# Kernel optimization log

Hardware: AMD Instinct MI355X
Metric: run time of the kernel (lower is better)

The kernel has to match this reference:

```python
import jax, jax.numpy as jnp
import numpy as np

D = 1024        # d_model
H = 16          # query heads
HKV = 4         # kv heads (GQA)
HD = D // H     # head dim = 64
MAX_T = 1024
EPS = 1e-6
CAP = 50.0      # logit softcap


def _rope_cache(max_t, hd):
    inv = 1.0 / (10000.0 ** (np.arange(0, hd, 2, dtype=np.float32) / hd))  # (hd/2,)
    t = np.arange(max_t, dtype=np.float32)
    f = np.outer(t, inv)                                                   # (max_t, hd/2)
    return jnp.asarray(np.cos(f)), jnp.asarray(np.sin(f))


def setup_inputs() -> dict:
    key = jax.random.key(0)
    ks = jax.random.split(key, 5)
    x = jax.random.normal(ks[0], (2, 64, 256, D), jnp.float32)  # (B,T,S,D)
    wq = jax.random.normal(ks[1], (D, H * HD), jnp.float32) * 0.02
    wk = jax.random.normal(ks[2], (D, HKV * HD), jnp.float32) * 0.02
    wv = jax.random.normal(ks[3], (D, HKV * HD), jnp.float32) * 0.02
    wo = jax.random.normal(ks[4], (H * HD, D), jnp.float32) * 0.02
    q_scale = jnp.ones((HD,), jnp.float32)  # QKNorm learnable gains
    k_scale = jnp.ones((HD,), jnp.float32)
    rope_cos, rope_sin = _rope_cache(MAX_T, HD)
    return {"x": x, "wq": wq, "wk": wk, "wv": wv, "wo": wo,
            "q_scale": q_scale, "k_scale": k_scale,
            "rope_cos": rope_cos, "rope_sin": rope_sin}


def _rmsnorm(v, scale):
    return v * jax.lax.rsqrt(jnp.mean(v * v, axis=-1, keepdims=True) + EPS) * scale


def reference(x, wq, wk, wv, wo, q_scale, k_scale, rope_cos, rope_sin):
    B, T, S, Dm = x.shape
    # fold spatial positions into batch: each position attends causally over time
    xt = x.transpose(0, 2, 1, 3).reshape(B * S, T, Dm)          # (N,T,D)
    q = (xt @ wq).reshape(B * S, T, H, HD)
    k = (xt @ wk).reshape(B * S, T, HKV, HD)
    v = (xt @ wv).reshape(B * S, T, HKV, HD)
    # QK-norm (RMSNorm over head_dim) before RoPE
    q = _rmsnorm(q, q_scale)
    k = _rmsnorm(k, k_scale)
    # 1D RoPE over temporal positions (split-half convention)
    cos = rope_cos[:T][None, :, None, :]                        # (1,T,1,HD/2)
    sin = rope_sin[:T][None, :, None, :]

    def rot(u):
        u1, u2 = jnp.split(u, 2, axis=-1)
        return jnp.concatenate([u1 * cos - u2 * sin, u1 * sin + u2 * cos], axis=-1)

    q = rot(q)
    k = rot(k)
    # GQA: expand kv heads to match query heads
    rep = H // HKV
    k = jnp.repeat(k, rep, axis=2)
    v = jnp.repeat(v, rep, axis=2)
    scores = jnp.einsum('nthd,nshd->nhts', q, k) / np.float32(np.sqrt(HD))
    scores = CAP * jnp.tanh(scores / CAP)                        # logit softcap
    causal = jnp.tril(jnp.ones((T, T), bool))
    scores = jnp.where(causal, scores, jnp.float32(-1e30))
    a = jax.nn.softmax(scores, axis=-1)
    o = jnp.einsum('nhts,nshd->nthd', a, v).reshape(B * S, T, H * HD) @ wo
    return o.reshape(B, S, T, Dm).transpose(0, 2, 1, 3)          # (B,T,S,D)
```

## Files before the change

### kernel.cpp

```cpp
#include <hip/hip_runtime.h>
#include <hip/hip_bf16.h>

#define DM   1024
#define NHQ  16
#define NKVH 4
#define HDIM 64
#define TTT  64
#define SSS  256
#define NBB  2
#define MROWS 32768

using short8 = __attribute__((ext_vector_type(8))) short;
using short4v = __attribute__((ext_vector_type(4))) short;
using f32x4  = __attribute__((ext_vector_type(4))) float;

__device__ __forceinline__ short f2bf(float f) {
  union { __hip_bfloat16 h; short s; } u;
  u.h = __float2bfloat16(f);
  return u.s;
}

__device__ __forceinline__ f32x4 mfma16(short8 a, short8 b, f32x4 c) {
  return __builtin_amdgcn_mfma_f32_16x16x32_bf16(a, b, c, 0, 0, 0);
}

__device__ __forceinline__ void gload_lds16(const void* g, void* l) {
  __builtin_amdgcn_global_load_lds(
      (const __attribute__((address_space(1))) void*)g,
      (__attribute__((address_space(3))) void*)l, 16, 0, 0);
}

__global__ __launch_bounds__(256) void k_wt(const float* __restrict__ w,
                                            short* __restrict__ wt, int cols) {
  __shared__ float tile[32][33];
  int ctiles = cols >> 5;
  int tj = blockIdx.x % ctiles;
  int td = blockIdx.x / ctiles;
  int lx = threadIdx.x & 31, ly = threadIdx.x >> 5;
  #pragma unroll
  for (int rr = 0; rr < 32; rr += 8)
    tile[rr + ly][lx] = w[(size_t)(td * 32 + rr + ly) * cols + tj * 32 + lx];
  __syncthreads();
  #pragma unroll
  for (int rr = 0; rr < 32; rr += 8)
    wt[(size_t)(tj * 32 + rr + ly) * 1024 + td * 32 + lx] = f2bf(tile[lx][rr + ly]);
}

#define GEMM256_8PH(Ab, Bb)                                                    \
  const int tid = threadIdx.x, lane = tid & 63, wid = tid >> 6;                \
  const int wr = wid >> 2, wc = wid & 3;                                       \
  const int ln15 = lane & 15, lhi = lane >> 4;                                 \
  const int rsw = ln15 & 7;                                                    \
  f32x4 acc[8][4] = {};                                                        \
  auto SHALF = [&](const short* gb, short* lb, int half, int kt) {             \
    _Pragma("unroll")                                                          \
    for (int i = 0; i < 2; ++i) {                                              \
      int c = i * 512 + tid;                                                   \
      int row = c >> 3, slot = c & 7;                                          \
      gload_lds16(gb + (size_t)(half * 128 + row) * 1024 + kt                  \
                     + ((slot ^ (row & 7)) << 3),                              \
                  lb + half * 8192 + c * 8);                                   \
    }                                                                          \
  };                                                                           \
  SHALF(Ab, sm, 0, 0); SHALF(Ab, sm, 1, 0);                                    \
  SHALF(Bb, sm + 16384, 0, 0); SHALF(Bb, sm + 16384, 1, 0);                    \
  SHALF(Ab, sm + 32768, 0, 64); SHALF(Ab, sm + 32768, 1, 64);                  \
  SHALF(Bb, sm + 49152, 0, 64); SHALF(Bb, sm + 49152, 1, 64);                  \
  asm volatile("s_waitcnt vmcnt(8)" ::: "memory");                             \
  __builtin_amdgcn_s_barrier();                                                \
  for (int g = 0; g < 16; ++g) {                                               \
    short* cA = sm + (g & 1) * 32768;                                          \
    short* cB = cA + 16384;                                                    \
    short* nA = sm + ((g + 1) & 1) * 32768;                                    \
    const bool iA = (g > 0) && (g < 15);                                       \
    const bool iB = (g < 14);                                                  \
    short8 a[4], b0[4], b1[4];                                                 \
    _Pragma("unroll")                                                          \
    for (int n = 0; n < 4; ++n)                                                \
      b0[n] = *(const short8*)(cB + (wc * 64 + n * 16 + ln15) * 64             \
                                  + ((lhi ^ rsw) << 3));                       \
    _Pragma("unroll")                                                          \
    for (int m = 0; m < 4; ++m)                                                \
      a[m] = *(const short8*)(cA + (wr * 128 + m * 16 + ln15) * 64             \
                                 + ((lhi ^ rsw) << 3));                        \
    if (iA) SHALF(Ab, nA, 0, (g + 1) * 64);                                    \
    __builtin_amdgcn_s_barrier();                                              \
    asm volatile("s_waitcnt lgkmcnt(0)" ::: "memory");                         \
    __builtin_amdgcn_s_setprio(1);                                             \
    _Pragma("unroll")                                                          \
    for (int m = 0; m < 4; ++m)                                                \
      _Pragma("unroll")                                                        \
      for (int n = 0; n < 4; ++n) acc[m][n] = mfma16(a[m], b0[n], acc[m][n]);  \
    __builtin_amdgcn_s_setprio(0);                                             \
    __builtin_amdgcn_s_barrier();                                              \
    _Pragma("unroll")                                                          \
    for (int m = 0; m < 4; ++m)                                                \
      a[m] = *(const short8*)(cA + (wr * 128 + 64 + m * 16 + ln15) * 64        \
                                 + ((lhi ^ rsw) << 3));                        \
    if (iA) SHALF(Ab, nA, 1, (g + 1) * 64);                                    \
    __builtin_amdgcn_s_barrier();                                              \
    asm volatile("s_waitcnt lgkmcnt(0)" ::: "memory");                         \
    __builtin_amdgcn_s_setprio(1);                                             \
    _Pragma("unroll")                                                          \
    for (int m = 0; m < 4; ++m)                                                \
      _Pragma("unroll")                                                        \
      for (int n = 0; n < 4; ++n)                                              \
        acc[4 + m][n] = mfma16(a[m], b0[n], acc[4 + m][n]);                    \
    __builtin_amdgcn_s_setprio(0);                                             \
    __builtin_amdgcn_s_barrier();                                              \
    _Pragma("unroll")                                                          \
    for (int n = 0; n < 4; ++n)                                                \
      b1[n] = *(const short8*)(cB + (wc * 64 + n * 16 + ln15) * 64             \
                                  + (((4 + lhi) ^ rsw) << 3));                 \
    _Pragma("unroll")                                                          \
    for (int m = 0; m < 4; ++m)                                                \
      a[m] = *(const short8*)(cA + (wr * 128 + m * 16 + ln15) * 64             \
                                 + (((4 + lhi) ^ rsw) << 3));                  \
    __builtin_amdgcn_s_barrier();                                              \
    asm volatile("s_waitcnt lgkmcnt(0)" ::: "memory");                         \
    __builtin_amdgcn_s_setprio(1);                                             \
    _Pragma("unroll")                                                          \
    for (int m = 0; m < 4; ++m)                                                \
      _Pragma("unroll")                                                        \
      for (int n = 0; n < 4; ++n) acc[m][n] = mfma16(a[m], b1[n], acc[m][n]);  \
    __builtin_amdgcn_s_setprio(0);                                             \
    __builtin_amdgcn_s_barrier();                                              \
    _Pragma("unroll")                                                          \
    for (int m = 0; m < 4; ++m)                                                \
      a[m] = *(const short8*)(cA + (wr * 128 + 64 + m * 16 + ln15) * 64        \
                                 + (((4 + lhi) ^ rsw) << 3));                  \
    if (iB) { SHALF(Bb, cB, 0, (g + 2) * 64); SHALF(Bb, cB, 1, (g + 2) * 64); }\
    __builtin_amdgcn_s_barrier();                                              \
    asm volatile("s_waitcnt lgkmcnt(0)" ::: "memory");                         \
    __builtin_amdgcn_s_setprio(1);                                             \
    _Pragma("unroll")                                                          \
    for (int m = 0; m < 4; ++m)                                                \
      _Pragma("unroll")                                                        \
      for (int n = 0; n < 4; ++n)                                              \
        acc[4 + m][n] = mfma16(a[m], b1[n], acc[4 + m][n]);                    \
    __builtin_amdgcn_s_setprio(0);                                             \
    if (g < 14)       asm volatile("s_waitcnt vmcnt(4)" ::: "memory");         \
    else if (g == 14) asm volatile("s_waitcnt vmcnt(0)" ::: "memory");         \
    __builtin_amdgcn_s_barrier();                                              \
  }

__global__ __launch_bounds__(512) void k_qkv(
    const float* __restrict__ x, const short* __restrict__ wt,
    const float* __restrict__ qscale, const float* __restrict__ kscale,
    const float* __restrict__ rcos, const float* __restrict__ rsin,
    short* __restrict__ qb, short* __restrict__ kb, short* __restrict__ vb) {
  __shared__ __align__(16) short sm[65536];
  const int bid = blockIdx.x;
  const int swz = (bid & 7) * 96 + (bid >> 3);
  const int tn = swz % 6, tm = swz / 6;
  const short* Bb = wt + (size_t)tn * 256 * 1024;
  const int tid = threadIdx.x, lane = tid & 63, wid = tid >> 6;
  const int wr = wid >> 2, wc = wid & 3;
  const int ln15 = lane & 15, lhi = lane >> 4;
  const int rsw = ln15 & 7;
  f32x4 acc[8][4] = {};
  const int arow = tid >> 3, aslot = tid & 7;
  const float* aptr[2][2];
  #pragma unroll
  for (int half = 0; half < 2; ++half)
    #pragma unroll
    for (int i = 0; i < 2; ++i) {
      int row = half * 128 + i * 64 + arow;
      int gr = tm * 256 + row;
      int nseq = gr >> 6, t = gr & 63;
      int b = nseq >> 8, s = nseq & 255;
      aptr[half][i] = x + ((size_t)((b * 64 + t) * 256 + s)) * 1024
                        + ((aslot ^ (row & 7)) << 3);
    }
  float4 ra[2][2][2], rb[2][2][2];
  auto A_ISSUE = [&](float4 (&rg)[2][2][2], int half, int kt) {
    #pragma unroll
    for (int i = 0; i < 2; ++i) {
      rg[half][i][0] = *(const float4*)(aptr[half][i] + kt);
      rg[half][i][1] = *(const float4*)(aptr[half][i] + kt + 4);
    }
  };
  auto A_WRITE = [&](float4 (&rg)[2][2][2], short* dA, int half) {
    #pragma unroll
    for (int i = 0; i < 2; ++i) {
      short8 v;
      #pragma unroll
      for (int e = 0; e < 4; ++e) {
        v[e]     = f2bf(rg[half][i][0][e]);
        v[4 + e] = f2bf(rg[half][i][1][e]);
      }
      *(short8*)(dA + half * 8192 + (i * 512 + tid) * 8) = v;
    }
  };
  auto BHALF = [&](short* lb, int half, int kt) {
    #pragma unroll
    for (int i = 0; i < 2; ++i) {
      int c = i * 512 + tid;
      int row = c >> 3, slot = c & 7;
      gload_lds16(Bb + (size_t)(half * 128 + row) * 1024 + kt
                     + ((slot ^ (row & 7)) << 3),
                  lb + half * 8192 + c * 8);
    }
  };
  A_ISSUE(ra, 0, 0); A_ISSUE(ra, 1, 0);
  BHALF(sm + 16384, 0, 0); BHALF(sm + 16384, 1, 0);
  A_ISSUE(rb, 0, 64); A_ISSUE(rb, 1, 64);
  BHALF(sm + 49152, 0, 64); BHALF(sm + 49152, 1, 64);
  asm volatile("s_waitcnt vmcnt(16)" ::: "memory");
  A_WRITE(ra, sm, 0); A_WRITE(ra, sm, 1);
  asm volatile("s_waitcnt vmcnt(4)" ::: "memory");
  A_WRITE(rb, sm + 32768, 0); A_WRITE(rb, sm + 32768, 1);
  asm volatile("s_waitcnt lgkmcnt(0)" ::: "memory");
  __builtin_amdgcn_s_barrier();
  for (int g = 0; g < 16; ++g) {
    short* cA = sm + (g & 1) * 32768;
    short* cB = cA + 16384;
    short* nA = sm + ((g + 1) & 1) * 32768;
    const bool iA = (g > 0) && (g < 15);
    const bool iB = (g < 14);
    short8 a[4], b0[4], b1[4];
    #pragma unroll
    for (int n = 0; n < 4; ++n)
      b0[n] = *(const short8*)(cB + (wc * 64 + n * 16 + ln15) * 64 + ((lhi ^ rsw) << 3));
    #pragma unroll
    for (int m = 0; m < 4; ++m)
      a[m] = *(const short8*)(cA + (wr * 128 + m * 16 + ln15) * 64 + ((lhi ^ rsw) << 3));
    if (iA) A_ISSUE(ra, 0, (g + 1) * 64);
    __builtin_amdgcn_s_barrier();
    asm volatile("s_waitcnt lgkmcnt(0)" ::: "memory");
    __builtin_amdgcn_s_setprio(1);
    #pragma unroll
    for (int m = 0; m < 4; ++m)
      #pragma unroll
      for (int n = 0; n < 4; ++n) acc[m][n] = mfma16(a[m], b0[n], acc[m][n]);
    __builtin_amdgcn_s_setprio(0);
    __builtin_amdgcn_s_barrier();
    #pragma unroll
    for (int m = 0; m < 4; ++m)
      a[m] = *(const short8*)(cA + (wr * 128 + 64 + m * 16 + ln15) * 64 + ((lhi ^ rsw) << 3));
    if (iA) A_ISSUE(ra, 1, (g + 1) * 64);
    __builtin_amdgcn_s_barrier();
    asm volatile("s_waitcnt lgkmcnt(0)" ::: "memory");
    __builtin_amdgcn_s_setprio(1);
    #pragma unroll
    for (int m = 0; m < 4; ++m)
      #pragma unroll
      for (int n = 0; n < 4; ++n) acc[4 + m][n] = mfma16(a[m], b0[n], acc[4 + m][n]);
    __builtin_amdgcn_s_setprio(0);
    __builtin_amdgcn_s_barrier();
    #pragma unroll
    for (int n = 0; n < 4; ++n)
      b1[n] = *(const short8*)(cB + (wc * 64 + n * 16 + ln15) * 64 + (((4 + lhi) ^ rsw) << 3));
    #pragma unroll
    for (int m = 0; m < 4; ++m)
      a[m] = *(const short8*)(cA + (wr * 128 + m * 16 + ln15) * 64 + (((4 + lhi) ^ rsw) << 3));
    if (iB) { BHALF(cB, 0, (g + 2) * 64); BHALF(cB, 1, (g + 2) * 64); }
    __builtin_amdgcn_s_barrier();
    asm volatile("s_waitcnt lgkmcnt(0)" ::: "memory");
    __builtin_amdgcn_s_setprio(1);
    #pragma unroll
    for (int m = 0; m < 4; ++m)
      #pragma unroll
      for (int n = 0; n < 4; ++n) acc[m][n] = mfma16(a[m], b1[n], acc[m][n]);
    __builtin_amdgcn_s_setprio(0);
    __builtin_amdgcn_s_barrier();
    #pragma unroll
    for (int m = 0; m < 4; ++m)
      a[m] = *(const short8*)(cA + (wr * 128 + 64 + m * 16 + ln15) * 64 + (((4 + lhi) ^ rsw) << 3));
    __builtin_amdgcn_s_barrier();
    asm volatile("s_waitcnt lgkmcnt(0)" ::: "memory");
    __builtin_amdgcn_s_setprio(1);
    #pragma unroll
    for (int m = 0; m < 4; ++m)
      #pragma unroll
      for (int n = 0; n < 4; ++n) acc[4 + m][n] = mfma16(a[m], b1[n], acc[4 + m][n]);
    __builtin_amdgcn_s_setprio(0);
    if (g < 14)       asm volatile("s_waitcnt vmcnt(4)" ::: "memory");
    else if (g == 14) asm volatile("s_waitcnt vmcnt(0)" ::: "memory");
    if (iA) {
      A_WRITE(ra, nA, 0); A_WRITE(ra, nA, 1);
      asm volatile("s_waitcnt lgkmcnt(0)" ::: "memory");
    }
    __builtin_amdgcn_s_barrier();
  }

  short* ot = sm;
  if (tn < 5) {
    const float* scale = (tn < 4) ? qscale : kscale;
    float sc[4];
    #pragma unroll
    for (int n = 0; n < 4; ++n) sc[n] = scale[n * 16 + ln15];
    #pragma unroll
    for (int m = 0; m < 8; ++m) {
      #pragma unroll
      for (int j = 0; j < 4; ++j) {
        float ss = 0.f;
        #pragma unroll
        for (int n = 0; n < 4; ++n) { float v = acc[m][n][j]; ss += v * v; }
        #pragma unroll
        for (int off = 8; off; off >>= 1) ss += __shfl_xor(ss, off, 64);
        float rms = rsqrtf(ss * (1.f / 64.f) + 1e-6f);
        int rl = wr * 128 + m * 16 + lhi * 4 + j;
        int t = (tm * 256 + rl) & 63;
        #pragma unroll
        for (int n = 0; n < 2; ++n) {
          int i = n * 16 + ln15;
          float cs = rcos[t * 32 + i], sn = rsin[t * 32 + i];
          float v1 = acc[m][n][j] * rms * sc[n];
          float v2 = acc[m][n + 2][j] * rms * sc[n + 2];
          ot[rl * 256 + wc * 64 + i]      = f2bf(v1 * cs - v2 * sn);
          ot[rl * 256 + wc * 64 + i + 32] = f2bf(v1 * sn + v2 * cs);
        }
      }
    }
  } else {
    #pragma unroll
    for (int m = 0; m < 8; ++m)
      #pragma unroll
      for (int n = 0; n < 4; ++n)
        #pragma unroll
        for (int j = 0; j < 4; ++j) {
          int rl = wr * 128 + m * 16 + lhi * 4 + j;
          ot[rl * 256 + wc * 64 + n * 16 + ln15] = f2bf(acc[m][n][j]);
        }
  }
  __syncthreads();
  {
    int row = tid >> 1, half = tid & 1;
    int r = tm * 256 + row;
    const uint4* src = (const uint4*)(ot + row * 256 + half * 128);
    short* dst;
    if (tn < 4)       dst = qb + (size_t)r * 1024 + tn * 256 + half * 128;
    else if (tn == 4) dst = kb + (size_t)r * 256 + half * 128;
    else              dst = vb + (size_t)r * 256 + half * 128;
    uint4* d4 = (uint4*)dst;
    #pragma unroll
    for (int i = 0; i < 16; ++i) d4[i] = src[i];
  }
}

__global__ __launch_bounds__(512) void k_attn(const short* __restrict__ qb,
                                              const short* __restrict__ kb,
                                              const short* __restrict__ vb,
                                              short* __restrict__ ob) {
  __shared__ __align__(16) short Vt[256 * 72];
  __shared__ __align__(16) short Ps[8][64 * 72];
  const int n = blockIdx.x;
  const int tid = threadIdx.x, lane = tid & 63, wid = tid >> 6;
  const int ln15 = lane & 15, lhi = lane >> 4;
  #pragma unroll
  for (int it = 0; it < 4; ++it) {
    int id = it * 512 + tid;
    int s = id >> 5, c8 = id & 31;
    short8 vv = *(const short8*)(vb + ((size_t)(n * 64 + s)) * 256 + c8 * 8);
    #pragma unroll
    for (int e = 0; e < 8; ++e) Vt[(c8 * 8 + e) * 72 + s] = vv[e];
  }
  __syncthreads();
  short* Pt = &Ps[wid][0];
  #pragma unroll
  for (int hh = 0; hh < 2; ++hh) {
    const int h = wid + hh * 8;
    const int kvh = h >> 2;
    short8 bk[4][2], aq[4][2];
    #pragma unroll
    for (int m = 0; m < 4; ++m)
      #pragma unroll
      for (int kk = 0; kk < 2; ++kk)
        bk[m][kk] = *(const short8*)(kb + ((size_t)(n * 64 + m * 16 + ln15)) * 256
                                        + kvh * 64 + kk * 32 + lhi * 8);
    #pragma unroll
    for (int nn = 0; nn < 4; ++nn)
      #pragma unroll
      for (int kk = 0; kk < 2; ++kk)
        aq[nn][kk] = *(const short8*)(qb + ((size_t)(n * 64 + nn * 16 + ln15)) * 1024
                                         + h * 64 + kk * 32 + lhi * 8);
    f32x4 sa[4][4] = {};
    __builtin_amdgcn_s_setprio(1);
    #pragma unroll
    for (int kk = 0; kk < 2; ++kk)
      #pragma unroll
      for (int m = 0; m < 4; ++m)
        #pragma unroll
        for (int nn = 0; nn < 4; ++nn)
          sa[m][nn] = mfma16(bk[m][kk], aq[nn][kk], sa[m][nn]);
    __builtin_amdgcn_s_setprio(0);
    #pragma unroll
    for (int m = 0; m < 4; ++m)
      #pragma unroll
      for (int nn = 0; nn < 4; ++nn)
        #pragma unroll
        for (int j = 0; j < 4; ++j) {
          float e2 = __expf(sa[m][nn][j] * 0.005f);
          float cap = 50.f * (e2 - 1.f) * __builtin_amdgcn_rcpf(e2 + 1.f);
          int scur = m * 16 + lhi * 4 + j, tcur = nn * 16 + ln15;
          sa[m][nn][j] = (scur <= tcur) ? cap : -1e30f;
        }
    float inv[4];
    #pragma unroll
    for (int nn = 0; nn < 4; ++nn) {
      float mx = -3e38f;
      #pragma unroll
      for (int m = 0; m < 4; ++m)
        #pragma unroll
        for (int j = 0; j < 4; ++j) mx = fmaxf(mx, sa[m][nn][j]);
      mx = fmaxf(mx, __shfl_xor(mx, 16, 64));
      mx = fmaxf(mx, __shfl_xor(mx, 32, 64));
      float sum = 0.f;
      #pragma unroll
      for (int m = 0; m < 4; ++m)
        #pragma unroll
        for (int j = 0; j < 4; ++j) {
          float e = __expf(sa[m][nn][j] - mx);
          sa[m][nn][j] = e; sum += e;
        }
      sum += __shfl_xor(sum, 16, 64);
      sum += __shfl_xor(sum, 32, 64);
      inv[nn] = __builtin_amdgcn_rcpf(sum);
    }
    #pragma unroll
    for (int nn = 0; nn < 4; ++nn)
      #pragma unroll
      for (int m = 0; m < 4; ++m) {
        short4v w;
        #pragma unroll
        for (int j = 0; j < 4; ++j) w[j] = f2bf(sa[m][nn][j] * inv[nn]);
        *(short4v*)(Pt + (nn * 16 + ln15) * 72 + m * 16 + lhi * 4) = w;
      }
    short8 ap[4][2], bv[4][2];
    #pragma unroll
    for (int m = 0; m < 4; ++m)
      #pragma unroll
      for (int kk = 0; kk < 2; ++kk)
        ap[m][kk] = *(const short8*)(Pt + (m * 16 + ln15) * 72 + kk * 32 + lhi * 8);
    #pragma unroll
    for (int nn = 0; nn < 4; ++nn)
      #pragma unroll
      for (int kk = 0; kk < 2; ++kk)
        bv[nn][kk] = *(const short8*)(&Vt[(kvh * 64 + nn * 16 + ln15) * 72 + kk * 32 + lhi * 8]);
    f32x4 oa[4][4] = {};
    __builtin_amdgcn_s_setprio(1);
    #pragma unroll
    for (int kk = 0; kk < 2; ++kk)
      #pragma unroll
      for (int m = 0; m < 4; ++m)
        #pragma unroll
        for (int nn = 0; nn < 4; ++nn)
          oa[m][nn] = mfma16(ap[m][kk], bv[nn][kk], oa[m][nn]);
    __builtin_amdgcn_s_setprio(0);
    #pragma unroll
    for (int m = 0; m < 4; ++m)
      #pragma unroll
      for (int nn = 0; nn < 4; ++nn)
        #pragma unroll
        for (int j = 0; j < 4; ++j)
          Pt[(m * 16 + lhi * 4 + j) * 72 + nn * 16 + ln15] = f2bf(oa[m][nn][j]);
    #pragma unroll
    for (int c = 0; c < 8; ++c)
      *(uint4*)(ob + ((size_t)(n * 64 + lane)) * 1024 + h * 64 + c * 8)
          = *(const uint4*)(Pt + lane * 72 + c * 8);
  }
}

__global__ __launch_bounds__(512, 2) void k_out(const short* __restrict__ ab,
                                                const short* __restrict__ wt,
                                                float* __restrict__ out) {
  __shared__ __align__(16) short sm[65536];
  const int bid = blockIdx.x;
  const int swz = (bid & 7) * 64 + (bid >> 3);
  const int tn = swz & 3, tm = swz >> 2;
  const short* Ab = ab + (size_t)tm * 256 * 1024;
  const short* Bb = wt + (size_t)tn * 256 * 1024;
  GEMM256_8PH(Ab, Bb)

  float* of = (float*)sm;
  #pragma unroll
  for (int ch = 0; ch < 2; ++ch) {
    if (wr == ch) {
      #pragma unroll
      for (int m = 0; m < 8; ++m)
        #pragma unroll
        for (int n = 0; n < 4; ++n)
          #pragma unroll
          for (int j = 0; j < 4; ++j)
            of[(m * 16 + lhi * 4 + j) * 256 + wc * 64 + n * 16 + ln15] = acc[m][n][j];
    }
    __syncthreads();
    {
      int row = tid >> 2, q4 = tid & 3;
      int r = tm * 256 + ch * 128 + row;
      int nseq = r >> 6, t = r & 63;
      int b = nseq >> 8, s = nseq & 255;
      float* dst = out + ((size_t)((b * TTT + t) * SSS + s)) * DM + tn * 256 + q4 * 64;
      const float4* src = (const float4*)(of + row * 256 + q4 * 64);
      float4* d4 = (float4*)dst;
      #pragma unroll
      for (int i = 0; i < 16; ++i) d4[i] = src[i];
    }
    __syncthreads();
  }
}

extern "C" void kernel_launch(void* const* d_in, const int* in_sizes, int n_in,
                              void* d_out, int out_size, void* d_ws, size_t ws_size,
                              hipStream_t stream) {
  const float* x  = (const float*)d_in[0];
  const float* wq = (const float*)d_in[1];
  const float* wk = (const float*)d_in[2];
  const float* wv = (const float*)d_in[3];
  const float* wo = (const float*)d_in[4];
  const float* qs = (const float*)d_in[5];
  const float* ks = (const float*)d_in[6];
  const float* rc = (const float*)d_in[7];
  const float* rs = (const float*)d_in[8];
  float* out = (float*)d_out;
  char* ws = (char*)d_ws;

  short* ob    = (short*)(ws);
  short* wqkvT = (short*)(ws + 67108864);
  short* woT   = (short*)(ws + 70254592);
  short* qb    = (short*)(ws + 72351744);
  short* kb    = (short*)(ws + 139460608);
  short* vb    = (short*)(ws + 156237824);

  k_wt<<<1024, 256, 0, stream>>>(wq, wqkvT, 1024);
  k_wt<<<256, 256, 0, stream>>>(wk, wqkvT + (size_t)1024 * 1024, 256);
  k_wt<<<256, 256, 0, stream>>>(wv, wqkvT + (size_t)1280 * 1024, 256);
  k_wt<<<1024, 256, 0, stream>>>(wo, woT, 1024);
  k_qkv<<<768, 512, 0, stream>>>(x, wqkvT, qs, ks, rc, rs, qb, kb, vb);
  k_attn<<<512, 512, 0, stream>>>(qb, kb, vb, ob);
  k_out<<<512, 512, 0, stream>>>(ob, woT, out);
}
```

Measured before the change: 356.8 us.

## Pre-convert x to bf16 in a separate pass and reuse shared GEMM macro

```diff
diff --git a/kernel.cpp b/kernel.cpp
--- a/kernel.cpp
+++ b/kernel.cpp
@@ -28,6 +28,19 @@
   __builtin_amdgcn_global_load_lds(
       (const __attribute__((address_space(1))) void*)g,
       (__attribute__((address_space(3))) void*)l, 16, 0, 0);
+}
+
+__global__ __launch_bounds__(256) void k_xconv(const float* __restrict__ x,
+                                               short* __restrict__ xb) {
+  int r = blockIdx.x;
+  int n = r >> 6, t = r & 63;
+  int b = n >> 8, s = n & 255;
+  const float4* src = (const float4*)(x + ((size_t)((b * TTT + t) * SSS + s)) * DM);
+  short4* dst = (short4*)(xb + (size_t)r * DM);
+  float4 v = src[threadIdx.x];
+  short4 o;
+  o.x = f2bf(v.x); o.y = f2bf(v.y); o.z = f2bf(v.z); o.w = f2bf(v.w);
+  dst[threadIdx.x] = o;
 }
 
 __global__ __launch_bounds__(256) void k_wt(const float* __restrict__ w,
@@ -144,8 +157,8 @@
     __builtin_amdgcn_s_barrier();                                              \
   }
 
-__global__ __launch_bounds__(512) void k_qkv(
-    const float* __restrict__ x, const short* __restrict__ wt,
+__global__ __launch_bounds__(512, 2) void k_qkv(
+    const short* __restrict__ xb, const short* __restrict__ wt,
     const float* __restrict__ qscale, const float* __restrict__ kscale,
     const float* __restrict__ rcos, const float* __restrict__ rsin,
     short* __restrict__ qb, short* __restrict__ kb, short* __restrict__ vb) {
@@ -153,136 +166,9 @@
   const int bid = blockIdx.x;
   const int swz = (bid & 7) * 96 + (bid >> 3);
   const int tn = swz % 6, tm = swz / 6;
+  const short* Ab = xb + (size_t)tm * 256 * 1024;
   const short* Bb = wt + (size_t)tn * 256 * 1024;
-  const int tid = threadIdx.x, lane = tid & 63, wid = tid >> 6;
-  const int wr = wid >> 2, wc = wid & 3;
-  const int ln15 = lane & 15, lhi = lane >> 4;
-  const int rsw = ln15 & 7;
-  f32x4 acc[8][4] = {};
-  const int arow = tid >> 3, aslot = tid & 7;
-  const float* aptr[2][2];
-  #pragma unroll
-  for (int half = 0; half < 2; ++half)
-    #pragma unroll
-    for (int i = 0; i < 2; ++i) {
-      int row = half * 128 + i * 64 + arow;
-      int gr = tm * 256 + row;
-      int nseq = gr >> 6, t = gr & 63;
-      int b = nseq >> 8, s = nseq & 255;
-      aptr[half][i] = x + ((size_t)((b * 64 + t) * 256 + s)) * 1024
-                        + ((aslot ^ (row & 7)) << 3);
-    }
-  float4 ra[2][2][2], rb[2][2][2];
-  auto A_ISSUE = [&](float4 (&rg)[2][2][2], int half, int kt) {
-    #pragma unroll
-    for (int i = 0; i < 2; ++i) {
-      rg[half][i][0] = *(const float4*)(aptr[half][i] + kt);
-      rg[half][i][1] = *(const float4*)(aptr[half][i] + kt + 4);
-    }
-  };
-  auto A_WRITE = [&](float4 (&rg)[2][2][2], short* dA, int half) {
-    #pragma unroll
-    for (int i = 0; i < 2; ++i) {
-      short8 v;
-      #pragma unroll
-      for (int e = 0; e < 4; ++e) {
-        v[e]     = f2bf(rg[half][i][0][e]);
-        v[4 + e] = f2bf(rg[half][i][1][e]);
-      }
-      *(short8*)(dA + half * 8192 + (i * 512 + tid) * 8) = v;
-    }
-  };
-  auto BHALF = [&](short* lb, int half, int kt) {
-    #pragma unroll
-    for (int i = 0; i < 2; ++i) {
-      int c = i * 512 + tid;
-      int row = c >> 3, slot = c & 7;
-      gload_lds16(Bb + (size_t)(half * 128 + row) * 1024 + kt
-                     + ((slot ^ (row & 7)) << 3),
-                  lb + half * 8192 + c * 8);
-    }
-  };
-  A_ISSUE(ra, 0, 0); A_ISSUE(ra, 1, 0);
-  BHALF(sm + 16384, 0, 0); BHALF(sm + 16384, 1, 0);
-  A_ISSUE(rb, 0, 64); A_ISSUE(rb, 1, 64);
-  BHALF(sm + 49152, 0, 64); BHALF(sm + 49152, 1, 64);
-  asm volatile("s_waitcnt vmcnt(16)" ::: "memory");
-  A_WRITE(ra, sm, 0); A_WRITE(ra, sm, 1);
-  asm volatile("s_waitcnt vmcnt(4)" ::: "memory");
-  A_WRITE(rb, sm + 32768, 0); A_WRITE(rb, sm + 32768, 1);
-  asm volatile("s_waitcnt lgkmcnt(0)" ::: "memory");
-  __builtin_amdgcn_s_barrier();
-  for (int g = 0; g < 16; ++g) {
-    short* cA = sm + (g & 1) * 32768;
-    short* cB = cA + 16384;
-    short* nA = sm + ((g + 1) & 1) * 32768;
-    const bool iA = (g > 0) && (g < 15);
-    const bool iB = (g < 14);
-    short8 a[4], b0[4], b1[4];
-    #pragma unroll
-    for (int n = 0; n < 4; ++n)
-      b0[n] = *(const short8*)(cB + (wc * 64 + n * 16 + ln15) * 64 + ((lhi ^ rsw) << 3));
-    #pragma unroll
-    for (int m = 0; m < 4; ++m)
-      a[m] = *(const short8*)(cA + (wr * 128 + m * 16 + ln15) * 64 + ((lhi ^ rsw) << 3));
-    if (iA) A_ISSUE(ra, 0, (g + 1) * 64);
-    __builtin_amdgcn_s_barrier();
-    asm volatile("s_waitcnt lgkmcnt(0)" ::: "memory");
-    __builtin_amdgcn_s_setprio(1);
-    #pragma unroll
-    for (int m = 0; m < 4; ++m)
-      #pragma unroll
-      for (int n = 0; n < 4; ++n) acc[m][n] = mfma16(a[m], b0[n], acc[m][n]);
-    __builtin_amdgcn_s_setprio(0);
-    __builtin_amdgcn_s_barrier();
-    #pragma unroll
-    for (int m = 0; m < 4; ++m)
-      a[m] = *(const short8*)(cA + (wr * 128 + 64 + m * 16 + ln15) * 64 + ((lhi ^ rsw) << 3));
-    if (iA) A_ISSUE(ra, 1, (g + 1) * 64);
-    __builtin_amdgcn_s_barrier();
-    asm volatile("s_waitcnt lgkmcnt(0)" ::: "memory");
-    __builtin_amdgcn_s_setprio(1);
-    #pragma unroll
-    for (int m = 0; m < 4; ++m)
-      #pragma unroll
-      for (int n = 0; n < 4; ++n) acc[4 + m][n] = mfma16(a[m], b0[n], acc[4 + m][n]);
-    __builtin_amdgcn_s_setprio(0);
-    __builtin_amdgcn_s_barrier();
-    #pragma unroll
-    for (int n = 0; n < 4; ++n)
-      b1[n] = *(const short8*)(cB + (wc * 64 + n * 16 + ln15) * 64 + (((4 + lhi) ^ rsw) << 3));
-    #pragma unroll
-    for (int m = 0; m < 4; ++m)
-      a[m] = *(const short8*)(cA + (wr * 128 + m * 16 + ln15) * 64 + (((4 + lhi) ^ rsw) << 3));
-    if (iB) { BHALF(cB, 0, (g + 2) * 64); BHALF(cB, 1, (g + 2) * 64); }
-    __builtin_amdgcn_s_barrier();
-    asm volatile("s_waitcnt lgkmcnt(0)" ::: "memory");
-    __builtin_amdgcn_s_setprio(1);
-    #pragma unroll
-    for (int m = 0; m < 4; ++m)
-      #pragma unroll
-      for (int n = 0; n < 4; ++n) acc[m][n] = mfma16(a[m], b1[n], acc[m][n]);
-    __builtin_amdgcn_s_setprio(0);
-    __builtin_amdgcn_s_barrier();
-    #pragma unroll
-    for (int m = 0; m < 4; ++m)
-      a[m] = *(const short8*)(cA + (wr * 128 + 64 + m * 16 + ln15) * 64 + (((4 + lhi) ^ rsw) << 3));
-    __builtin_amdgcn_s_barrier();
-    asm volatile("s_waitcnt lgkmcnt(0)" ::: "memory");
-    __builtin_amdgcn_s_setprio(1);
-    #pragma unroll
-    for (int m = 0; m < 4; ++m)
-      #pragma unroll
-      for (int n = 0; n < 4; ++n) acc[4 + m][n] = mfma16(a[m], b1[n], acc[4 + m][n]);
-    __builtin_amdgcn_s_setprio(0);
-    if (g < 14)       asm volatile("s_waitcnt vmcnt(4)" ::: "memory");
-    else if (g == 14) asm volatile("s_waitcnt vmcnt(0)" ::: "memory");
-    if (iA) {
-      A_WRITE(ra, nA, 0); A_WRITE(ra, nA, 1);
-      asm volatile("s_waitcnt lgkmcnt(0)" ::: "memory");
-    }
-    __builtin_amdgcn_s_barrier();
-  }
+  GEMM256_8PH(Ab, Bb)
 
   short* ot = sm;
   if (tn < 5) {
@@ -516,18 +402,20 @@
   float* out = (float*)d_out;
   char* ws = (char*)d_ws;
 
-  short* ob    = (short*)(ws);
+  short* xb    = (short*)(ws);
   short* wqkvT = (short*)(ws + 67108864);
   short* woT   = (short*)(ws + 70254592);
   short* qb    = (short*)(ws + 72351744);
   short* kb    = (short*)(ws + 139460608);
   short* vb    = (short*)(ws + 156237824);
-
+  short* ob    = xb;
+
+  k_xconv<<<MROWS, 256, 0, stream>>>(x, xb);
   k_wt<<<1024, 256, 0, stream>>>(wq, wqkvT, 1024);
   k_wt<<<256, 256, 0, stream>>>(wk, wqkvT + (size_t)1024 * 1024, 256);
   k_wt<<<256, 256, 0, stream>>>(wv, wqkvT + (size_t)1280 * 1024, 256);
   k_wt<<<1024, 256, 0, stream>>>(wo, woT, 1024);
-  k_qkv<<<768, 512, 0, stream>>>(x, wqkvT, qs, ks, rc, rs, qb, kb, vb);
+  k_qkv<<<768, 512, 0, stream>>>(xb, wqkvT, qs, ks, rc, rs, qb, kb, vb);
   k_attn<<<512, 512, 0, stream>>>(qb, kb, vb, ob);
   k_out<<<512, 512, 0, stream>>>(ob, woT, out);
 }
```

Measured after the change: 342.9 us. 3.9% less time.
